# Optimization experiments

Measured on AMD Instinct MI355X. Metric: run time of the kernel, lower is better.

Reference implementation:

```python
import jax, jax.numpy as jnp
import numpy as np

N_BINS = 20  # matches init kwarg n_bins


def setup_inputs() -> dict:
    key = jax.random.key(0)
    k1, k2 = jax.random.split(key)
    preds = jax.random.uniform(k1, (16, 1024, 1024), dtype=jnp.float32)
    targets = jax.random.uniform(k2, (16, 1024, 1024), dtype=jnp.float32)
    return {"preds": preds, "targets": targets}


def reference(preds, targets):
    # Single-pass scatter histogram replacing the original per-bin mask loop.
    p = preds.reshape(-1)
    t = targets.reshape(-1).astype(jnp.float32)
    # torch loop: element belongs to bin i iff bins[i] <= p < bins[i+1];
    # p outside [0,1) (e.g. exactly 1.0) falls in no bin.
    idx = jnp.clip(jnp.floor(p * N_BINS).astype(jnp.int32), 0, N_BINS - 1)
    w = ((p >= 0.0) & (p < 1.0)).astype(p.dtype)  # in-range indicator (constant wrt grads)
    cnt = jax.ops.segment_sum(w, idx, num_segments=N_BINS)           # per-bin counts
    sum_p = jax.ops.segment_sum(p * w, idx, num_segments=N_BINS)     # per-bin sum of confidences
    sum_t = jax.ops.segment_sum(t * w, idx, num_segments=N_BINS)     # per-bin sum of accuracies
    valid = cnt > 0
    safe_cnt = jnp.where(valid, cnt, 1.0)
    per_bin = jnp.abs(sum_p / safe_cnt - sum_t / safe_cnt)
    n_valid = jnp.sum(valid.astype(p.dtype))
    ace = jnp.sum(jnp.where(valid, per_bin, 0.0)) / jnp.maximum(n_valid, 1.0)
    return ace
```

## Files before the change

### kernel.cpp

```cpp
#include <hip/hip_runtime.h>

#define NBINS 20
#define NQ (3 * NBINS)
#define BT 128

__global__ __launch_bounds__(BT) void ace_partial(
    const float4* __restrict__ preds4, const float4* __restrict__ targs4,
    const float* __restrict__ preds, const float* __restrict__ targs,
    float* __restrict__ partials, int nvec, int n, int nblocks)
{
    __shared__ float4 hist[NBINS][BT];
    const int tid = threadIdx.x;

    #pragma unroll
    for (int b = 0; b < NBINS; ++b)
        hist[b][tid] = make_float4(0.f, 0.f, 0.f, 0.f);
    __syncthreads();

    const int stride = gridDim.x * BT;
    int i = blockIdx.x * BT + tid;

    if (i < nvec) {
        float4 pa = preds4[i];
        float4 ta = targs4[i];
        for (;;) {
            const int j = i + stride;
            const bool hasNext = j < nvec;
            float4 pb, tb;
            if (hasNext) { pb = preds4[j]; tb = targs4[j]; }

            const float pv[4] = {pa.x, pa.y, pa.z, pa.w};
            const float tv[4] = {ta.x, ta.y, ta.z, ta.w};
            #pragma unroll
            for (int e = 0; e < 4; ++e) {
                const float p = pv[e];
                int b = (int)(p * (float)NBINS);
                b = b < 0 ? 0 : (b > NBINS - 1 ? NBINS - 1 : b);
                const float w = (p >= 0.0f && p < 1.0f) ? 1.0f : 0.0f;
                float4 h = hist[b][tid];
                h.x += w;
                h.y += p * w;
                h.z += tv[e] * w;
                hist[b][tid] = h;
            }

            if (!hasNext) break;
            pa = pb; ta = tb; i = j;
        }
    }

    if (blockIdx.x == 0 && tid == 0) {
        for (int r = nvec * 4; r < n; ++r) {
            const float p = preds[r];
            int b = (int)(p * (float)NBINS);
            b = b < 0 ? 0 : (b > NBINS - 1 ? NBINS - 1 : b);
            const float w = (p >= 0.0f && p < 1.0f) ? 1.0f : 0.0f;
            float4 h = hist[b][0];
            h.x += w; h.y += p * w; h.z += targs[r] * w;
            hist[b][0] = h;
        }
    }
    __syncthreads();

    if (tid < NQ) {
        const int b = tid / 3, c = tid % 3;
        float s = 0.0f;
        for (int t = 0; t < BT; ++t) {
            const float4 h = hist[b][t];
            s += (c == 0) ? h.x : (c == 1) ? h.y : h.z;
        }
        partials[(size_t)(c * NBINS + b) * nblocks + blockIdx.x] = s;
    }
}

__global__ __launch_bounds__(1024) void ace_final(
    const float* __restrict__ partials, float* __restrict__ out, int nblocks)
{
    __shared__ double sums[NQ];
    const int t = threadIdx.x;
    const int q = t >> 4;
    const int l = t & 15;

    if (q < NQ) {
        double s = 0.0;
        const float* src = partials + (size_t)q * nblocks;
        for (int b = l; b < nblocks; b += 16)
            s += (double)src[b];
        #pragma unroll
        for (int off = 8; off; off >>= 1)
            s += __shfl_down(s, off, 16);
        if (l == 0) sums[q] = s;
    }
    __syncthreads();

    if (t == 0) {
        double ace = 0.0;
        int nvalid = 0;
        for (int b = 0; b < NBINS; ++b) {
            const double cnt = sums[b];
            if (cnt > 0.0) {
                ++nvalid;
                ace += fabs(sums[NBINS + b] / cnt - sums[2 * NBINS + b] / cnt);
            }
        }
        out[0] = (float)(ace / (double)(nvalid > 0 ? nvalid : 1));
    }
}

extern "C" void kernel_launch(void* const* d_in, const int* in_sizes, int n_in,
                              void* d_out, int out_size, void* d_ws, size_t ws_size,
                              hipStream_t stream)
{
    const float* preds = (const float*)d_in[0];
    const float* targs = (const float*)d_in[1];
    const int n = in_sizes[0];
    const int nvec = n / 4;

    int nblocks = 1024;
    const size_t need = (size_t)NQ * nblocks * sizeof(float);
    if (need > ws_size) {
        nblocks = (int)(ws_size / (NQ * sizeof(float)));
        if (nblocks < 1) nblocks = 1;
    }

    float* partials = (float*)d_ws;
    ace_partial<<<nblocks, BT, 0, stream>>>(
        (const float4*)preds, (const float4*)targs, preds, targs,
        partials, nvec, n, nblocks);
    ace_final<<<1, 1024, 0, stream>>>(partials, (float*)d_out, nblocks);
}
```

Measured before the change: 174.7 us.

## Split shared histogram into planar arrays, tree-reduce, and atomically accumulate global sums

The per-thread shared histogram moves from float4 bins to three planar float arrays, so each update is three scalar LDS accesses instead of a float4 load and store. The serial per-column block reduction becomes a parallel tree reduction, and block results go to 60 global sums through atomicAdd instead of a partials buffer. This removes the big final reduction kernel and raises the grid to 1280 blocks, at the cost of a memset launch, float rather than double accumulation in the final step, and nondeterministic atomic ordering.

```diff
diff --git a/kernel.cpp b/kernel.cpp
--- a/kernel.cpp
+++ b/kernel.cpp
@@ -7,15 +7,19 @@
 __global__ __launch_bounds__(BT) void ace_partial(
     const float4* __restrict__ preds4, const float4* __restrict__ targs4,
     const float* __restrict__ preds, const float* __restrict__ targs,
-    float* __restrict__ partials, int nvec, int n, int nblocks)
+    float* __restrict__ gsums, int nvec, int n)
 {
-    __shared__ float4 hist[NBINS][BT];
+    __shared__ float hist[NQ * BT];
     const int tid = threadIdx.x;
 
     #pragma unroll
-    for (int b = 0; b < NBINS; ++b)
-        hist[b][tid] = make_float4(0.f, 0.f, 0.f, 0.f);
+    for (int q = 0; q < NQ; ++q)
+        hist[q * BT + tid] = 0.0f;
     __syncthreads();
+
+    float* hc = &hist[(0 * NBINS) * BT + tid];
+    float* hp = &hist[(1 * NBINS) * BT + tid];
+    float* ht = &hist[(2 * NBINS) * BT + tid];
 
     const int stride = gridDim.x * BT;
     int i = blockIdx.x * BT + tid;
@@ -37,11 +41,10 @@
                 int b = (int)(p * (float)NBINS);
                 b = b < 0 ? 0 : (b > NBINS - 1 ? NBINS - 1 : b);
                 const float w = (p >= 0.0f && p < 1.0f) ? 1.0f : 0.0f;
-                float4 h = hist[b][tid];
-                h.x += w;
-                h.y += p * w;
-                h.z += tv[e] * w;
-                hist[b][tid] = h;
+                const int o = b * BT;
+                hc[o] += w;
+                hp[o] += p * w;
+                ht[o] += tv[e] * w;
             }
 
             if (!hasNext) break;
@@ -55,56 +58,48 @@
             int b = (int)(p * (float)NBINS);
             b = b < 0 ? 0 : (b > NBINS - 1 ? NBINS - 1 : b);
             const float w = (p >= 0.0f && p < 1.0f) ? 1.0f : 0.0f;
-            float4 h = hist[b][0];
-            h.x += w; h.y += p * w; h.z += targs[r] * w;
-            hist[b][0] = h;
+            const int o = b * BT;
+            hc[o] += w;
+            hp[o] += p * w;
+            ht[o] += targs[r] * w;
+        }
+    }
+
+    #pragma unroll
+    for (int s = BT / 2; s >= 1; s >>= 1) {
+        __syncthreads();
+        for (int k = tid; k < NQ * s; k += BT) {
+            const int q = k / s, c = k - q * s;
+            hist[q * BT + c] += hist[q * BT + c + s];
         }
     }
     __syncthreads();
 
-    if (tid < NQ) {
-        const int b = tid / 3, c = tid % 3;
-        float s = 0.0f;
-        for (int t = 0; t < BT; ++t) {
-            const float4 h = hist[b][t];
-            s += (c == 0) ? h.x : (c == 1) ? h.y : h.z;
-        }
-        partials[(size_t)(c * NBINS + b) * nblocks + blockIdx.x] = s;
-    }
+    if (tid < NQ)
+        atomicAdd(&gsums[tid], hist[tid * BT]);
 }
 
-__global__ __launch_bounds__(1024) void ace_final(
-    const float* __restrict__ partials, float* __restrict__ out, int nblocks)
+__global__ __launch_bounds__(64) void ace_final(
+    const float* __restrict__ gsums, float* __restrict__ out)
 {
-    __shared__ double sums[NQ];
-    const int t = threadIdx.x;
-    const int q = t >> 4;
-    const int l = t & 15;
-
-    if (q < NQ) {
-        double s = 0.0;
-        const float* src = partials + (size_t)q * nblocks;
-        for (int b = l; b < nblocks; b += 16)
-            s += (double)src[b];
-        #pragma unroll
-        for (int off = 8; off; off >>= 1)
-            s += __shfl_down(s, off, 16);
-        if (l == 0) sums[q] = s;
+    const int l = threadIdx.x;
+    float per = 0.0f, valid = 0.0f;
+    if (l < NBINS) {
+        const float cnt = gsums[l];
+        const float sp  = gsums[NBINS + l];
+        const float st  = gsums[2 * NBINS + l];
+        if (cnt > 0.0f) {
+            valid = 1.0f;
+            per = fabsf(sp / cnt - st / cnt);
+        }
     }
-    __syncthreads();
-
-    if (t == 0) {
-        double ace = 0.0;
-        int nvalid = 0;
-        for (int b = 0; b < NBINS; ++b) {
-            const double cnt = sums[b];
-            if (cnt > 0.0) {
-                ++nvalid;
-                ace += fabs(sums[NBINS + b] / cnt - sums[2 * NBINS + b] / cnt);
-            }
-        }
-        out[0] = (float)(ace / (double)(nvalid > 0 ? nvalid : 1));
+    #pragma unroll
+    for (int off = 32; off; off >>= 1) {
+        per   += __shfl_down(per, off);
+        valid += __shfl_down(valid, off);
     }
+    if (l == 0)
+        out[0] = per / fmaxf(valid, 1.0f);
 }
 
 extern "C" void kernel_launch(void* const* d_in, const int* in_sizes, int n_in,
@@ -116,16 +111,12 @@
     const int n = in_sizes[0];
     const int nvec = n / 4;
 
-    int nblocks = 1024;
-    const size_t need = (size_t)NQ * nblocks * sizeof(float);
-    if (need > ws_size) {
-        nblocks = (int)(ws_size / (NQ * sizeof(float)));
-        if (nblocks < 1) nblocks = 1;
-    }
+    float* gsums = (float*)d_ws;
+    hipMemsetAsync(gsums, 0, NQ * sizeof(float), stream);
 
-    float* partials = (float*)d_ws;
+    const int nblocks = 1280;
     ace_partial<<<nblocks, BT, 0, stream>>>(
         (const float4*)preds, (const float4*)targs, preds, targs,
-        partials, nvec, n, nblocks);
-    ace_final<<<1, 1024, 0, stream>>>(partials, (float*)d_out, nblocks);
+        gsums, nvec, n);
+    ace_final<<<1, 64, 0, stream>>>(gsums, (float*)d_out);
 }
```

Result: no change. 173.0 us (-1.0%).
